# Performance work log

Hardware: AMD Instinct MI355X
Metric: run time of the kernel (lower is better)

## Reference

```python
import jax, jax.numpy as jnp
import numpy as np
from jax import lax

W_WIN = 7  # window size from init_kwargs


def _dwconv(x, k):
    """Depthwise 2D conv, SAME padding, kernel k: [C,1,kh,kw] (OIHW)."""
    C = x.shape[1]
    p = k.shape[-1] // 2
    return lax.conv_general_dilated(
        x, k, window_strides=(1, 1), padding=[(p, p), (p, p)],
        feature_group_count=C, dimension_numbers=("NCHW", "OIHW", "NCHW"))


def setup_inputs() -> dict:
    key = jax.random.key(0)
    ks = jax.random.split(key, 6)
    B, C, H, Wd = 1, 48, 56, 56
    x = jax.random.normal(ks[0], (B, C, H, Wd), dtype=jnp.float32)
    # small init scale keeps the softmax logits (dot/49) in a sane range
    w3 = jax.random.normal(ks[1], (C, 1, 3, 3), dtype=jnp.float32) * 0.1
    w5 = jax.random.normal(ks[2], (C, 1, 5, 5), dtype=jnp.float32) * 0.1
    w7 = jax.random.normal(ks[3], (C, 1, 7, 7), dtype=jnp.float32) * 0.1
    pw = jax.random.normal(ks[4], (C, 3 * C, 1, 1), dtype=jnp.float32) * 0.05
    pb = jax.random.normal(ks[5], (C,), dtype=jnp.float32) * 0.01
    return {"x": x, "w3": w3, "w5": w5, "w7": w7, "pw": pw, "pb": pb}


def reference(x, w3, w5, w7, pw, pb):
    B, C, H, Wd = x.shape
    w = W_WIN
    # multi-scale depthwise branch, concat on channels -> [B, 3C, H, W]
    y = jnp.concatenate([_dwconv(x, w3), _dwconv(x, w5), _dwconv(x, w7)], axis=1)
    pad_h = (-H) % w
    pad_w = (-Wd) % w
    if pad_h or pad_w:  # static Python ints -> jit-safe
        y = jnp.pad(y, ((0, 0), (0, 0), (0, pad_h), (0, pad_w)), mode="reflect")
    Hp, Wp = y.shape[2], y.shape[3]
    nH, nW = Hp // w, Wp // w
    C3 = 3 * C
    # equivalent to torch unfold(2,w,w).unfold(3,w,w).permute(0,1,2,4,3,5)
    # .reshape(B,3C,nH*nW,w*w): same row-major linearization
    yw = y.reshape(B, C3, nH * nW, w * w)
    # rows: (B, nH*nW, 3C) flattened -> N x (w*w)
    yf = yw.transpose(0, 2, 1, 3).reshape(B * nH * nW * C3, w * w)
    # full N x N self-attention over all rows (faithful to the original)
    attn = jax.nn.softmax((yf @ yf.T) / (w * w), axis=-1)
    y_hat = (attn @ yf).reshape(B, nH, nW, C3, w, w)
    y_hat = y_hat.transpose(0, 3, 1, 4, 2, 5).reshape(B, C3, nH * w, nW * w)
    y_hat = y_hat[:, :, :H, :Wd]
    # 1x1 projection 3C -> C, plus residual
    out = jnp.einsum("oi,bihw->bohw", pw[:, :, 0, 0], y_hat) + pb[None, :, None, None]
    return x + out
```

## Files before the change

### kernel.cpp

```cpp
#include <hip/hip_runtime.h>

typedef unsigned int uint;
typedef unsigned short ushort;
typedef __attribute__((ext_vector_type(8))) short bf16x8;
typedef __attribute__((ext_vector_type(4))) float f32x4;
typedef __attribute__((ext_vector_type(8))) unsigned short ushort8v;

#define C_IN   48
#define C3     144
#define HW     56
#define SSP    3136
#define DW     49
#define DPAD   64
#define NROWS  9216

#define NSPLIT 12
#define TPS    12

#define CSC 0.02944245f

#define YF_B    0
#define YFT_B   1179648
#define OPART_B 2359296
#define ESUM_B  (OPART_B + NSPLIT * DW * NROWS * 2)


__device__ __forceinline__ ushort f32_to_bf16_rne(float x) {
  uint b = __float_as_uint(x);
  b += 0x7fffu + ((b >> 16) & 1u);
  return (ushort)(b >> 16);
}
__device__ __forceinline__ float bf16_to_f32(ushort u) {
  return __uint_as_float(((uint)u) << 16);
}
__device__ __forceinline__ void async_copy16(const void* g, void* l) {
  __builtin_amdgcn_global_load_lds(
      (const __attribute__((address_space(1))) unsigned int*)g,
      (__attribute__((address_space(3))) unsigned int*)l, 16, 0, 0);
}

template <int KS>
__device__ __forceinline__ float dwconv_val(const float* __restrict__ xc,
                                            const float* __restrict__ wk,
                                            int h, int w, bool interior) {
  constexpr int P = KS / 2;
  float val = 0.f;
  if (interior) {
#pragma unroll
    for (int dy = 0; dy < KS; dy++) {
      const float* xr = xc + (h + dy - P) * HW;
      const float* wr = wk + dy * KS;
#pragma unroll
      for (int dx = 0; dx < KS; dx++)
        val += xr[w + dx - P] * wr[dx];
    }
  } else {
#pragma unroll
    for (int dy = 0; dy < KS; dy++) {
      int hy = h + dy - P;
      if (hy < 0 || hy >= HW) continue;
      const float* xr = xc + hy * HW;
      const float* wr = wk + dy * KS;
#pragma unroll
      for (int dx = 0; dx < KS; dx++) {
        int wx = w + dx - P;
        if (wx < 0 || wx >= HW) continue;
        val += xr[wx] * wr[dx];
      }
    }
  }
  return val;
}

__global__ __launch_bounds__(256) void conv_kernel(
    const float* __restrict__ x, const float* __restrict__ w3,
    const float* __restrict__ w5, const float* __restrict__ w7,
    ushort* __restrict__ yf, ushort* __restrict__ yfT) {
  __shared__ ushort tile[4][64];
  const int tid = threadIdx.x;
  const int idx = blockIdx.x * 256 + tid;
  const int r = idx >> 6, t = idx & 63;
  const int rr = r & 3;
  const int r0 = r & ~3;

  ushort ov = 0;
  if (t < DW) {
    int g = r / C3, c3 = r - g * C3;
    int flat = g * DW + t;
    int h = flat / HW, w = flat - h * HW;
    int grp = c3 / C_IN, c = c3 - grp * C_IN;
    int nh = g >> 3, nw = g & 7;
    bool interior = ((uint)(nh - 1) <= 5u) && ((uint)(nw - 1) <= 5u);
    const float* xc = x + c * SSP;
    float val;
    if (grp == 0)      val = dwconv_val<3>(xc, w3 + c * 9,  h, w, interior);
    else if (grp == 1) val = dwconv_val<5>(xc, w5 + c * 25, h, w, interior);
    else               val = dwconv_val<7>(xc, w7 + c * 49, h, w, interior);
    ov = f32_to_bf16_rne(val);
  }
  yf[idx] = ov;
  tile[rr][t] = ov;
  __syncthreads();

  if (tid < 64) {
    ushort4 v;
    if (tid == 56) {
      v.x = 0x3F80; v.y = 0x3F80; v.z = 0x3F80; v.w = 0x3F80;
    } else {
      v.x = tile[0][tid]; v.y = tile[1][tid];
      v.z = tile[2][tid]; v.w = tile[3][tid];
    }
    const int k6 = r0 & 63;
    const int pcol = (r0 & ~63) | (k6 & 35) | ((k6 & 12) << 1) | ((k6 & 16) >> 2);
    *(ushort4*)&yfT[tid * NROWS + pcol] = v;
  }
}

__global__ __launch_bounds__(512, 4) void attn_kernel(
    const ushort* __restrict__ yf, const ushort* __restrict__ yfT,
    ushort* __restrict__ opart, float* __restrict__ esum_g) {
  __shared__ __align__(16) char smem[32768];

  const int tid = threadIdx.x;
  const int w = tid >> 6, lane = tid & 63;
  const int q = lane >> 4, c = lane & 15;
  const int m0 = blockIdx.x * 256 + w * 32;
  const int sp = blockIdx.y;

  bf16x8 qf[2][2];
#pragma unroll
  for (int mt = 0; mt < 2; mt++)
#pragma unroll
    for (int ds = 0; ds < 2; ds++) {
      bf16x8 raw = *(const bf16x8*)&yf[(m0 + mt * 16 + c) * 64 + ds * 32 + q * 8];
      short tmp[8];
#pragma unroll
      for (int j = 0; j < 8; j++)
        tmp[j] = (short)f32_to_bf16_rne(bf16_to_f32((ushort)raw[j]) * CSC);
      qf[mt][ds] = *(bf16x8*)tmp;
    }

  f32x4 o[4][2];
#pragma unroll
  for (int dt = 0; dt < 4; dt++)
#pragma unroll
    for (int mt = 0; mt < 2; mt++) o[dt][mt] = (f32x4)0.f;

  {
    const int k0 = (sp * TPS) * 64;
    async_copy16(yf + (k0 + lane) * 64 + w * 8, smem + w * 1024);
    async_copy16(yfT + lane * NROWS + k0 + w * 8, smem + 16384 + w * 1024);
  }
  __syncthreads();

  for (int it = 0; it < TPS; it++) {
    const int cur = it & 1;
    if (it + 1 < TPS) {
      const int k1 = (sp * TPS + it + 1) * 64;
      async_copy16(yf + (k1 + lane) * 64 + w * 8,
                   smem + (cur ^ 1) * 8192 + w * 1024);
      async_copy16(yfT + lane * NROWS + k1 + w * 8,
                   smem + 16384 + (cur ^ 1) * 8192 + w * 1024);
    }

    const char* Kb = smem + cur * 8192;
    const char* Vb = smem + 16384 + cur * 8192;

    __builtin_amdgcn_s_setprio(1);

    bf16x8 bp[2][2];
#pragma unroll
    for (int nc = 0; nc < 2; nc++) {
      f32x4 s[2][2];
#pragma unroll
      for (int h = 0; h < 2; h++) {
        const int nt = nc * 2 + h;
        bf16x8 a0 = *(const bf16x8*)(Kb + q * 1024 + (nt * 16 + c) * 16);
        bf16x8 a1 = *(const bf16x8*)(Kb + (4 + q) * 1024 + (nt * 16 + c) * 16);
#pragma unroll
        for (int mt = 0; mt < 2; mt++) {
          f32x4 acc = (f32x4)0.f;
          acc = __builtin_amdgcn_mfma_f32_16x16x32_bf16(a0, qf[mt][0], acc, 0, 0, 0);
          acc = __builtin_amdgcn_mfma_f32_16x16x32_bf16(a1, qf[mt][1], acc, 0, 0, 0);
          s[h][mt] = acc;
        }
      }
#pragma unroll
      for (int mt = 0; mt < 2; mt++) {
        uint u00 = __float_as_uint(__builtin_amdgcn_exp2f(s[0][mt][0]));
        uint u01 = __float_as_uint(__builtin_amdgcn_exp2f(s[0][mt][1]));
        uint u02 = __float_as_uint(__builtin_amdgcn_exp2f(s[0][mt][2]));
        uint u03 = __float_as_uint(__builtin_amdgcn_exp2f(s[0][mt][3]));
        uint u10 = __float_as_uint(__builtin_amdgcn_exp2f(s[1][mt][0]));
        uint u11 = __float_as_uint(__builtin_amdgcn_exp2f(s[1][mt][1]));
        uint u12 = __float_as_uint(__builtin_amdgcn_exp2f(s[1][mt][2]));
        uint u13 = __float_as_uint(__builtin_amdgcn_exp2f(s[1][mt][3]));
        uint4 t4;
        t4.x = (u00 >> 16) | (u01 & 0xffff0000u);
        t4.y = (u02 >> 16) | (u03 & 0xffff0000u);
        t4.z = (u10 >> 16) | (u11 & 0xffff0000u);
        t4.w = (u12 >> 16) | (u13 & 0xffff0000u);
        bp[mt][nc] = *(bf16x8*)&t4;
      }
    }

#pragma unroll
    for (int dt = 0; dt < 4; dt++) {
      bf16x8 v0 = *(const bf16x8*)(Vb + q * 1024 + (dt * 16 + c) * 16);
      bf16x8 v1 = *(const bf16x8*)(Vb + (4 + q) * 1024 + (dt * 16 + c) * 16);
      o[dt][0] = __builtin_amdgcn_mfma_f32_16x16x32_bf16(v0, bp[0][0], o[dt][0], 0, 0, 0);
      o[dt][1] = __builtin_amdgcn_mfma_f32_16x16x32_bf16(v0, bp[1][0], o[dt][1], 0, 0, 0);
      o[dt][0] = __builtin_amdgcn_mfma_f32_16x16x32_bf16(v1, bp[0][1], o[dt][0], 0, 0, 0);
      o[dt][1] = __builtin_amdgcn_mfma_f32_16x16x32_bf16(v1, bp[1][1], o[dt][1], 0, 0, 0);
    }

    __builtin_amdgcn_s_setprio(0);

    if (it + 1 < TPS) __syncthreads();
  }

#pragma unroll
  for (int dt = 0; dt < 4; dt++)
#pragma unroll
    for (int mt = 0; mt < 2; mt++)
#pragma unroll
      for (int r = 0; r < 4; r++) {
        int d = dt * 16 + q * 4 + r;
        int m = m0 + mt * 16 + c;
        float v = o[dt][mt][r];
        if (d < DW) {
          opart[(sp * DW + d) * NROWS + m] = f32_to_bf16_rne(v);
        } else if (d == 56) {
          esum_g[sp * NROWS + m] = v;
        }
      }
}

__global__ __launch_bounds__(256) void fuse_pw_kernel(
    const ushort* __restrict__ opart, const float* __restrict__ esum_g,
    const float* __restrict__ x, const float* __restrict__ pw,
    const float* __restrict__ pb, float* __restrict__ out) {
  __shared__ float vb[7 * 145];
  __shared__ float inv_es[144];
  const int g = blockIdx.x, tch = blockIdx.y;
  const int t0 = tch * 7;
  const int tid = threadIdx.x;

  if (tid < 144) {
    int r = g * C3 + tid;
    float e = 0.f;
#pragma unroll
    for (int sp = 0; sp < NSPLIT; sp++) e += esum_g[sp * NROWS + r];
    inv_es[tid] = 1.f / e;
  }
  __syncthreads();

  for (int j = tid; j < 7 * 18; j += 256) {
    int tt = j / 18, ch = j - tt * 18;
    int i0 = ch * 8;
    int t = t0 + tt;
    float acc[8];
#pragma unroll
    for (int k = 0; k < 8; k++) acc[k] = 0.f;
#pragma unroll
    for (int sp = 0; sp < NSPLIT; sp++) {
      ushort8v v = *(const ushort8v*)&opart[(sp * DW + t) * NROWS + g * C3 + i0];
#pragma unroll
      for (int k = 0; k < 8; k++) acc[k] += bf16_to_f32(v[k]);
    }
#pragma unroll
    for (int k = 0; k < 8; k++)
      vb[tt * 145 + i0 + k] = acc[k] * inv_es[i0 + k];
  }
  __syncthreads();

  for (int j = tid; j < C_IN * 7; j += 256) {
    int o = j / 7, tt = j - o * 7;
    int t = t0 + tt;
    const float* pwo = pw + o * C3;
    const float* vrow = &vb[tt * 145];
    float a0 = 0.f, a1 = 0.f, a2 = 0.f, a3 = 0.f;
#pragma unroll
    for (int i = 0; i < C3; i += 4) {
      float4 wv = *(const float4*)&pwo[i];
      a0 += wv.x * vrow[i];
      a1 += wv.y * vrow[i + 1];
      a2 += wv.z * vrow[i + 2];
      a3 += wv.w * vrow[i + 3];
    }
    float acc = (a0 + a1) + (a2 + a3);
    int nh = g >> 3, nw = g & 7;
    int th = t / 7, tw = t - th * 7;
    int oidx = o * SSP + (nh * 7 + th) * HW + (nw * 7 + tw);
    out[oidx] = x[oidx] + pb[o] + acc;
  }
}

extern "C" void kernel_launch(void* const* d_in, const int* in_sizes, int n_in,
                              void* d_out, int out_size, void* d_ws, size_t ws_size,
                              hipStream_t stream) {
  const float* x  = (const float*)d_in[0];
  const float* w3 = (const float*)d_in[1];
  const float* w5 = (const float*)d_in[2];
  const float* w7 = (const float*)d_in[3];
  const float* pw = (const float*)d_in[4];
  const float* pb = (const float*)d_in[5];
  float* out = (float*)d_out;
  char* ws = (char*)d_ws;

  ushort* yf    = (ushort*)(ws + YF_B);
  ushort* yfT   = (ushort*)(ws + YFT_B);
  ushort* opart = (ushort*)(ws + OPART_B);
  float*  esum  = (float*)(ws + ESUM_B);

  conv_kernel<<<(NROWS * DPAD) / 256, 256, 0, stream>>>(x, w3, w5, w7, yf, yfT);
  attn_kernel<<<dim3(NROWS / 256, NSPLIT), 512, 0, stream>>>(yf, yfT, opart, esum);
  fuse_pw_kernel<<<dim3(64, 7), 256, 0, stream>>>(opart, esum, x, pw, pb, out);
}
```

Measured before the change: 111.1 us.

## Process two key tiles per barrier with a four-slot LDS ring

The attention kernel's shared buffer grows from 32KB to 64KB and now holds four K/V tile slots. Two tiles are prefetched per step, and each loop iteration handles two 64-row key tiles before one __syncthreads, halving the number of barriers. The cost is doubled LDS use per block, which can lower how many blocks fit on a CU and cut occupancy relative to the launch bound of 4.

```diff
diff --git a/kernel.cpp b/kernel.cpp
--- a/kernel.cpp
+++ b/kernel.cpp
@@ -119,13 +119,14 @@
 __global__ __launch_bounds__(512, 4) void attn_kernel(
     const ushort* __restrict__ yf, const ushort* __restrict__ yfT,
     ushort* __restrict__ opart, float* __restrict__ esum_g) {
-  __shared__ __align__(16) char smem[32768];
+  __shared__ __align__(16) char smem[65536];
 
   const int tid = threadIdx.x;
   const int w = tid >> 6, lane = tid & 63;
   const int q = lane >> 4, c = lane & 15;
   const int m0 = blockIdx.x * 256 + w * 32;
   const int sp = blockIdx.y;
+  const int base = sp * TPS;
 
   bf16x8 qf[2][2];
 #pragma unroll
@@ -147,76 +148,89 @@
     for (int mt = 0; mt < 2; mt++) o[dt][mt] = (f32x4)0.f;
 
   {
-    const int k0 = (sp * TPS) * 64;
+    const int k0 = base * 64;
     async_copy16(yf + (k0 + lane) * 64 + w * 8, smem + w * 1024);
-    async_copy16(yfT + lane * NROWS + k0 + w * 8, smem + 16384 + w * 1024);
+    async_copy16(yfT + lane * NROWS + k0 + w * 8, smem + 32768 + w * 1024);
+    const int k1 = (base + 1) * 64;
+    async_copy16(yf + (k1 + lane) * 64 + w * 8, smem + 8192 + w * 1024);
+    async_copy16(yfT + lane * NROWS + k1 + w * 8,
+                 smem + 32768 + 8192 + w * 1024);
   }
   __syncthreads();
 
-  for (int it = 0; it < TPS; it++) {
-    const int cur = it & 1;
-    if (it + 1 < TPS) {
-      const int k1 = (sp * TPS + it + 1) * 64;
-      async_copy16(yf + (k1 + lane) * 64 + w * 8,
-                   smem + (cur ^ 1) * 8192 + w * 1024);
-      async_copy16(yfT + lane * NROWS + k1 + w * 8,
-                   smem + 16384 + (cur ^ 1) * 8192 + w * 1024);
-    }
-
-    const char* Kb = smem + cur * 8192;
-    const char* Vb = smem + 16384 + cur * 8192;
-
-    __builtin_amdgcn_s_setprio(1);
-
-    bf16x8 bp[2][2];
-#pragma unroll
-    for (int nc = 0; nc < 2; nc++) {
-      f32x4 s[2][2];
-#pragma unroll
-      for (int h = 0; h < 2; h++) {
-        const int nt = nc * 2 + h;
-        bf16x8 a0 = *(const bf16x8*)(Kb + q * 1024 + (nt * 16 + c) * 16);
-        bf16x8 a1 = *(const bf16x8*)(Kb + (4 + q) * 1024 + (nt * 16 + c) * 16);
+  for (int jp = 0; jp < TPS / 2; jp++) {
+    if (jp + 1 < TPS / 2) {
+      const int t2 = 2 * jp + 2, t3 = 2 * jp + 3;
+      const int k2 = (base + t2) * 64;
+      const int k3 = (base + t3) * 64;
+      async_copy16(yf + (k2 + lane) * 64 + w * 8,
+                   smem + (t2 & 3) * 8192 + w * 1024);
+      async_copy16(yfT + lane * NROWS + k2 + w * 8,
+                   smem + 32768 + (t2 & 3) * 8192 + w * 1024);
+      async_copy16(yf + (k3 + lane) * 64 + w * 8,
+                   smem + (t3 & 3) * 8192 + w * 1024);
+      async_copy16(yfT + lane * NROWS + k3 + w * 8,
+                   smem + 32768 + (t3 & 3) * 8192 + w * 1024);
+    }
+
+#pragma unroll
+    for (int half = 0; half < 2; half++) {
+      const int it = 2 * jp + half;
+      const char* Kb = smem + (it & 3) * 8192;
+      const char* Vb = smem + 32768 + (it & 3) * 8192;
+
+      __builtin_amdgcn_s_setprio(1);
+
+      bf16x8 bp[2][2];
+#pragma unroll
+      for (int nc = 0; nc < 2; nc++) {
+        f32x4 s[2][2];
+#pragma unroll
+        for (int h = 0; h < 2; h++) {
+          const int nt = nc * 2 + h;
+          bf16x8 a0 = *(const bf16x8*)(Kb + q * 1024 + (nt * 16 + c) * 16);
+          bf16x8 a1 = *(const bf16x8*)(Kb + (4 + q) * 1024 + (nt * 16 + c) * 16);
+#pragma unroll
+          for (int mt = 0; mt < 2; mt++) {
+            f32x4 acc = (f32x4)0.f;
+            acc = __builtin_amdgcn_mfma_f32_16x16x32_bf16(a0, qf[mt][0], acc, 0, 0, 0);
+            acc = __builtin_amdgcn_mfma_f32_16x16x32_bf16(a1, qf[mt][1], acc, 0, 0, 0);
+            s[h][mt] = acc;
+          }
+        }
 #pragma unroll
         for (int mt = 0; mt < 2; mt++) {
-          f32x4 acc = (f32x4)0.f;
-          acc = __builtin_amdgcn_mfma_f32_16x16x32_bf16(a0, qf[mt][0], acc, 0, 0, 0);
-          acc = __builtin_amdgcn_mfma_f32_16x16x32_bf16(a1, qf[mt][1], acc, 0, 0, 0);
-          s[h][mt] = acc;
+          uint u00 = __float_as_uint(__builtin_amdgcn_exp2f(s[0][mt][0]));
+          uint u01 = __float_as_uint(__builtin_amdgcn_exp2f(s[0][mt][1]));
+          uint u02 = __float_as_uint(__builtin_amdgcn_exp2f(s[0][mt][2]));
+          uint u03 = __float_as_uint(__builtin_amdgcn_exp2f(s[0][mt][3]));
+          uint u10 = __float_as_uint(__builtin_amdgcn_exp2f(s[1][mt][0]));
+          uint u11 = __float_as_uint(__builtin_amdgcn_exp2f(s[1][mt][1]));
+          uint u12 = __float_as_uint(__builtin_amdgcn_exp2f(s[1][mt][2]));
+          uint u13 = __float_as_uint(__builtin_amdgcn_exp2f(s[1][mt][3]));
+          uint4 t4;
+          t4.x = (u00 >> 16) | (u01 & 0xffff0000u);
+          t4.y = (u02 >> 16) | (u03 & 0xffff0000u);
+          t4.z = (u10 >> 16) | (u11 & 0xffff0000u);
+          t4.w = (u12 >> 16) | (u13 & 0xffff0000u);
+          bp[mt][nc] = *(bf16x8*)&t4;
         }
       }
-#pragma unroll
-      for (int mt = 0; mt < 2; mt++) {
-        uint u00 = __float_as_uint(__builtin_amdgcn_exp2f(s[0][mt][0]));
-        uint u01 = __float_as_uint(__builtin_amdgcn_exp2f(s[0][mt][1]));
-        uint u02 = __float_as_uint(__builtin_amdgcn_exp2f(s[0][mt][2]));
-        uint u03 = __float_as_uint(__builtin_amdgcn_exp2f(s[0][mt][3]));
-        uint u10 = __float_as_uint(__builtin_amdgcn_exp2f(s[1][mt][0]));
-        uint u11 = __float_as_uint(__builtin_amdgcn_exp2f(s[1][mt][1]));
-        uint u12 = __float_as_uint(__builtin_amdgcn_exp2f(s[1][mt][2]));
-        uint u13 = __float_as_uint(__builtin_amdgcn_exp2f(s[1][mt][3]));
-        uint4 t4;
-        t4.x = (u00 >> 16) | (u01 & 0xffff0000u);
-        t4.y = (u02 >> 16) | (u03 & 0xffff0000u);
-        t4.z = (u10 >> 16) | (u11 & 0xffff0000u);
-        t4.w = (u12 >> 16) | (u13 & 0xffff0000u);
-        bp[mt][nc] = *(bf16x8*)&t4;
+
+#pragma unroll
+      for (int dt = 0; dt < 4; dt++) {
+        bf16x8 v0 = *(const bf16x8*)(Vb + q * 1024 + (dt * 16 + c) * 16);
+        bf16x8 v1 = *(const bf16x8*)(Vb + (4 + q) * 1024 + (dt * 16 + c) * 16);
+        o[dt][0] = __builtin_amdgcn_mfma_f32_16x16x32_bf16(v0, bp[0][0], o[dt][0], 0, 0, 0);
+        o[dt][1] = __builtin_amdgcn_mfma_f32_16x16x32_bf16(v0, bp[1][0], o[dt][1], 0, 0, 0);
+        o[dt][0] = __builtin_amdgcn_mfma_f32_16x16x32_bf16(v1, bp[0][1], o[dt][0], 0, 0, 0);
+        o[dt][1] = __builtin_amdgcn_mfma_f32_16x16x32_bf16(v1, bp[1][1], o[dt][1], 0, 0, 0);
       }
-    }
-
-#pragma unroll
-    for (int dt = 0; dt < 4; dt++) {
-      bf16x8 v0 = *(const bf16x8*)(Vb + q * 1024 + (dt * 16 + c) * 16);
-      bf16x8 v1 = *(const bf16x8*)(Vb + (4 + q) * 1024 + (dt * 16 + c) * 16);
-      o[dt][0] = __builtin_amdgcn_mfma_f32_16x16x32_bf16(v0, bp[0][0], o[dt][0], 0, 0, 0);
-      o[dt][1] = __builtin_amdgcn_mfma_f32_16x16x32_bf16(v0, bp[1][0], o[dt][1], 0, 0, 0);
-      o[dt][0] = __builtin_amdgcn_mfma_f32_16x16x32_bf16(v1, bp[0][1], o[dt][0], 0, 0, 0);
-      o[dt][1] = __builtin_amdgcn_mfma_f32_16x16x32_bf16(v1, bp[1][1], o[dt][1], 0, 0, 0);
-    }
-
-    __builtin_amdgcn_s_setprio(0);
-
-    if (it + 1 < TPS) __syncthreads();
+
+      __builtin_amdgcn_s_setprio(0);
+    }
+
+    if (jp + 1 < TPS / 2) __syncthreads();
   }
 
 #pragma unroll
```

Result: no change. 113.0 us (+1.8%).
